# Kernel optimization log

Hardware: AMD Instinct MI355X
Metric: run time of the kernel (lower is better)

The kernel has to match this reference:

```python
import jax, jax.numpy as jnp
import numpy as np
from jax import lax

B, D, H, W, C = 2, 144, 64, 160, 32
P = 300000
EPS = 1e-4   # scn BatchNormLeakyReLU default eps
LEAK = 0.2


def setup_inputs() -> dict:
    key = jax.random.key(0)
    ks = jax.random.split(key, 10)
    features = jax.random.normal(ks[0], (P, C), jnp.float32)
    b = jax.random.randint(ks[1], (P, 1), 0, B)
    x = jax.random.randint(ks[2], (P, 1), 0, D)
    y = jax.random.randint(ks[3], (P, 1), 0, H)
    z = jax.random.randint(ks[4], (P, 1), 0, W)
    coords = jnp.concatenate([b, x, y, z], axis=1).astype(jnp.int32)

    def conv_w(k, cin, cout):
        return jax.random.normal(k, (2, 2, 2, cin, cout), jnp.float32) / np.float32(np.sqrt(8 * cin))

    return {
        "features": features, "coords": coords,
        "w1": conv_w(ks[5], C, 64),  "g1": jnp.ones((64,), jnp.float32),  "b1": jnp.zeros((64,), jnp.float32),
        "w2": conv_w(ks[6], 64, 96), "g2": jnp.ones((96,), jnp.float32),  "b2": jnp.zeros((96,), jnp.float32),
        "w3": conv_w(ks[7], 96, 128),"g3": jnp.ones((128,), jnp.float32), "b3": jnp.zeros((128,), jnp.float32),
        "w4": conv_w(ks[8], 128, 1),
    }


def _densify(features, coords):
    # scn.InputLayer mode=4: average features of duplicate coordinates.
    lin = ((coords[:, 0] * D + coords[:, 1]) * H + coords[:, 2]) * W + coords[:, 3]
    grid = jnp.zeros((B * D * H * W, C), features.dtype).at[lin].add(features)
    cnt = jnp.zeros((B * D * H * W,), features.dtype).at[lin].add(1.0)
    grid = grid / jnp.maximum(cnt, 1.0)[:, None]
    x = grid.reshape(B, D, H, W, C)
    mask = (cnt > 0).astype(features.dtype).reshape(B, D, H, W, 1)
    return x, mask


def _conv2s2(x, w):
    # scn.Convolution(dim=3, filter=2, stride=2, bias=False): inactive inputs are zero,
    # so dense VALID conv reproduces values at active output sites exactly.
    return lax.conv_general_dilated(x, w, (2, 2, 2), 'VALID',
                                    dimension_numbers=('NDHWC', 'DHWIO', 'NDHWC'))


def _downsample_mask(mask):
    # Output site is active iff any input in its 2x2x2 window is active.
    return lax.reduce_window(mask, 0.0, lax.max, (1, 2, 2, 2, 1), (1, 2, 2, 2, 1), 'VALID')


def _block(x, mask, w, gamma, beta):
    x = _conv2s2(x, w)
    mask = _downsample_mask(mask)
    n = jnp.maximum(jnp.sum(mask), 1.0)
    # x is exactly zero at inactive sites, so sums over all sites == sums over active sites.
    mean = jnp.sum(x, axis=(0, 1, 2, 3)) / n
    var = jnp.sum(x * x, axis=(0, 1, 2, 3)) / n - mean * mean
    y = (x - mean) * (gamma * lax.rsqrt(var + EPS)) + beta
    y = jnp.where(y > 0, y, LEAK * y) * mask   # LeakyReLU on active sites, zero elsewhere
    return y, mask


def reference(features, coords, w1, g1, b1, w2, g2, b2, w3, g3, b3, w4):
    x, mask = _densify(features, coords)
    x, mask = _block(x, mask, w1, g1, b1)
    x, mask = _block(x, mask, w2, g2, b2)
    x, mask = _block(x, mask, w3, g3, b3)
    x = _conv2s2(x, w4)                 # [B, 9, 4, 10, 1]
    mask = _downsample_mask(mask)
    return jax.nn.sigmoid(x) * mask     # sigmoid of features; inactive sites zeroed
```

## Files before the change

kernel.cpp:

```cpp
#include <hip/hip_runtime.h>
#include <math.h>

#define PNUM 300000
#define B_ 2
#define D0 144
#define H0 64
#define W0 160
#define NVOX (B_*D0*H0*W0)

#define D1 72
#define H1 32
#define W1 80
#define N1S (B_*D1*H1*W1)

#define D2 36
#define H2 16
#define W2 40
#define N2S (B_*D2*H2*W2)

#define D3 18
#define H3 8
#define W3 20
#define N3S (B_*D3*H3*W3)

#define D4 9
#define H4 4
#define W4 10
#define N4S (B_*D4*H4*W4)

#define EPS_ 1e-4f
#define LEAK_ 0.2f

typedef __attribute__((ext_vector_type(8))) short v8s;
typedef __attribute__((ext_vector_type(4))) float v4f;

typedef unsigned short ushort_t;
typedef unsigned int uint_t;
typedef unsigned long long ull_t;

__device__ __forceinline__ ushort_t f2b(float f) {
  union { float f; uint_t u; } x; x.f = f;
  uint_t r = x.u + 0x7FFFu + ((x.u >> 16) & 1u);
  return (ushort_t)(r >> 16);
}
__device__ __forceinline__ float b2f(ushort_t h) {
  union { uint_t u; float f; } x; x.u = ((uint_t)h) << 16; return x.f;
}
__device__ __forceinline__ uint_t bn2(uint_t w, float s0, float h0, float s1, float h1,
                                      float msk) {
  float v0 = b2f((ushort_t)(w & 0xffff));
  float v1 = b2f((ushort_t)(w >> 16));
  v0 = fmaf(v0, s0, h0); v1 = fmaf(v1, s1, h1);
  v0 = fmaxf(v0, LEAK_ * v0) * msk;
  v1 = fmaxf(v1, LEAK_ * v1) * msk;
  return (uint_t)f2b(v0) | ((uint_t)f2b(v1) << 16);
}

template <int DD, int HH, int WW>
__device__ __forceinline__ int okey(int p) {
  int b = p / (DD*HH*WW); int r = p - b*(DD*HH*WW);
  int x = r / (HH*WW); r -= x*(HH*WW);
  int y = r / WW; int z = r - y*WW;
  return (((((b*(DD/2) + (x >> 1))*(HH/2) + (y >> 1))*(WW/2)) + (z >> 1)) << 3)
         | ((x & 1) << 2) | ((y & 1) << 1) | (z & 1);
}

#define OFF_CNT     0
#define OFF_STATS   2949120
#define OFF_CURSOR  2965504
#define OFF_SORTED  5914624
#define OFF_AKLIST  6214624
#define OFF_WT1     6514624
#define OFF_WT2     6522816
#define OFF_WT3     6555584
#define OFF_AFEATB  6621120
#define OFF_X1B     11421120
#define OFF_X2B     23217600
#define OFF_X3B     26166720
#define OFF_M1      26535360
#define OFF_M2      26904000
#define OFF_M3      26950080

#define ST_S1P  0
#define ST_Q1P  2560
#define ST_S2P  5120
#define ST_Q2P  7424
#define ST_S3P  9728
#define ST_Q3P  12032
#define ST_N2P  14336
#define ST_N3P  14368
#define ST_GCUR 14400
#define ST_PK   14404

__device__ __forceinline__ int voxkey(int b, int x, int y, int z) {
  int p = ((b*D1 + (x >> 1))*H1 + (y >> 1))*W1 + (z >> 1);
  int oct = ((x & 1) << 2) | ((y & 1) << 1) | (z & 1);
  return p*8 + oct;
}

#define NB_COUNT 1172
#define NB_PREPW 832
#define NB_STZ   16
__global__ __launch_bounds__(256) void k_front(
    const int* __restrict__ coords, int* __restrict__ cnt,
    const float* __restrict__ w1, const float* __restrict__ w2,
    const float* __restrict__ w3,
    ushort_t* __restrict__ wt1, ushort_t* __restrict__ wt2,
    ushort_t* __restrict__ wt3, float* __restrict__ stz) {
  int bb = blockIdx.x, t = threadIdx.x;
  if (bb < NB_COUNT) {
    int i = bb * 256 + t;
    if (i < PNUM) {
      int4 c = *(const int4*)(coords + i*4);
      atomicAdd(&cnt[voxkey(c.x, c.y, c.z, c.w)], 1);
    }
  } else if (bb < NB_COUNT + NB_PREPW) {
    int idx = (bb - NB_COUNT) * 256 + t;
    if (idx < 16384) {
      int c = idx >> 11, r = idx & 2047;
      int co = r >> 5, kk = r & 31;
      wt1[idx] = f2b(w1[(c*32 + kk)*64 + co]);
    } else if (idx < 16384 + 65536) {
      int i = idx - 16384;
      int c = i >> 12, r = i & 4095;
      int co = r >> 5, kk = r & 31;
      int k = c*32 + kk;
      wt2[i] = (co < 96) ? f2b(w2[k*96 + co]) : 0;
    } else {
      int i = idx - 81920;
      int c = i >> 12, r = i & 4095;
      int co = r >> 5, kk = r & 31;
      int k = c*32 + kk;
      int ch = k >> 7, ci = k & 127;
      wt3[i] = (ci < 96) ? f2b(w3[(ch*96 + ci)*128 + co]) : 0;
    }
  } else {
    int off = ((bb - NB_COUNT - NB_PREPW) * 256 + t) * 4;
    *(float4*)(stz + off) = make_float4(0.f, 0.f, 0.f, 0.f);
  }
}

__global__ __launch_bounds__(1024) void k_alloc(const int* __restrict__ cnt,
                                                int* __restrict__ cursor,
                                                float* __restrict__ m1b,
                                                int* __restrict__ aklist,
                                                int* __restrict__ gcur,
                                                ull_t* __restrict__ pkctr) {
  __shared__ ull_t wsum[16];
  __shared__ int slotBase;
  __shared__ ull_t pkBase;
  int t = threadIdx.x;
  int idx0 = blockIdx.x * 16384 + t * 16;
  int c[16];
  int tsum = 0;
#pragma unroll
  for (int j = 0; j < 4; j++) {
    int4 cv = *(const int4*)(cnt + idx0 + j*4);
    c[j*4+0] = cv.x; c[j*4+1] = cv.y; c[j*4+2] = cv.z; c[j*4+3] = cv.w;
    tsum += cv.x + cv.y + cv.z + cv.w;
  }
  uint_t m0 = 0, m1m = 0;
#pragma unroll
  for (int j = 0; j < 8; j++) { if (c[j] > 0) m0 |= (1u << j); }
#pragma unroll
  for (int j = 0; j < 8; j++) { if (c[8+j] > 0) m1m |= (1u << j); }
  int ck = __popc(m0) + __popc(m1m);
  int pa = ((m0 != 0) ? 1 : 0) + ((m1m != 0) ? 1 : 0);
  ull_t sv = ((ull_t)(uint_t)tsum << 32) | (ull_t)(uint_t)((pa << 16) | ck);
  int lane = t & 63, wid = t >> 6;
  ull_t incl = sv;
#pragma unroll
  for (int o = 1; o < 64; o <<= 1) {
    ull_t v = __shfl_up(incl, o);
    if (lane >= o) incl += v;
  }
  if (lane == 63) wsum[wid] = incl;
  __syncthreads();
  if (t == 0) {
    ull_t tot = 0;
#pragma unroll
    for (int w = 0; w < 16; w++) { ull_t v = wsum[w]; wsum[w] = tot; tot += v; }
    slotBase = atomicAdd(gcur, (int)(tot >> 32));
    uint_t pk = (uint_t)(tot & 0xffffffffULL);
    pkBase = atomicAdd(pkctr, ((ull_t)(pk >> 16) << 32) | (ull_t)(pk & 0xffff));
  }
  __syncthreads();
  ull_t excl = wsum[wid] + incl - sv;
  int st = slotBase + (int)(excl >> 32);
  uint_t pkl = (uint_t)(excl & 0xffffffffULL);
  int koff = (int)(pkBase & 0xffffffffULL) + (int)(pkl & 0xffff);
#pragma unroll
  for (int j = 0; j < 4; j++) {
    int4 sv2;
    sv2.x = st; st += c[j*4+0];
    sv2.y = st; st += c[j*4+1];
    sv2.z = st; st += c[j*4+2];
    sv2.w = st; st += c[j*4+3];
    *(int4*)(cursor + idx0 + j*4) = sv2;
  }
  int p0 = idx0 >> 3;
  m1b[okey<D1,H1,W1>(p0)]     = (m0 != 0) ? 1.f : 0.f;
  m1b[okey<D1,H1,W1>(p0 + 1)] = (m1m != 0) ? 1.f : 0.f;
  uint_t m = m0;
  while (m) { int i = __ffs(m) - 1; m &= m - 1; aklist[koff++] = p0*8 + i; }
  m = m1m;
  while (m) { int i = __ffs(m) - 1; m &= m - 1; aklist[koff++] = (p0 + 1)*8 + i; }
}

__global__ __launch_bounds__(256) void k_scatter(const int* __restrict__ coords,
                                                 int* __restrict__ cursor,
                                                 int* __restrict__ sorted) {
  int i = blockIdx.x * 256 + threadIdx.x;
  if (i >= PNUM) return;
  int4 c = *(const int4*)(coords + i*4);
  int slot = atomicAdd(&cursor[voxkey(c.x, c.y, c.z, c.w)], 1);
  sorted[slot] = i;
}

__global__ __launch_bounds__(256) void k_avg(const float* __restrict__ feat,
                                             const int* __restrict__ sorted,
                                             const int* __restrict__ cnt,
                                             const int* __restrict__ cursor,
                                             const int* __restrict__ aklist,
                                             const int* __restrict__ nactk,
                                             ushort_t* __restrict__ afb) {
  int gid = blockIdx.x * 256 + threadIdx.x;
  int j = gid >> 3;
  if (j >= nactk[0]) return;
  int key = aklist[j];
  int c = cnt[key];
  int s0 = cursor[key] - c;
  int q = (gid & 7) * 4;
  float4 acc = {0.f, 0.f, 0.f, 0.f};
  for (int i = 0; i < c; i++) {
    float4 v = *(const float4*)(feat + (size_t)sorted[s0 + i] * 32 + q);
    acc.x += v.x; acc.y += v.y; acc.z += v.z; acc.w += v.w;
  }
  float inv = 1.f / (float)c;
  uint2 o;
  o.x = (uint_t)f2b(acc.x*inv) | ((uint_t)f2b(acc.y*inv) << 16);
  o.y = (uint_t)f2b(acc.z*inv) | ((uint_t)f2b(acc.w*inv) << 16);
  *(uint2*)(afb + (size_t)s0 * 32 + q) = o;
}

__global__ __launch_bounds__(256) void k_conv1m(
    const ushort_t* __restrict__ afb, const int* __restrict__ cnt,
    const int* __restrict__ cursor, const ushort_t* __restrict__ wtg,
    ushort_t* __restrict__ x1b, float* __restrict__ sp, float* __restrict__ qp) {
  __shared__ __align__(16) ushort_t wlds[16384];
  __shared__ int cst[128*9];
  __shared__ int okl[128];
  __shared__ float redS[4][64], redQ[4][64];
  int t = threadIdx.x;
#pragma unroll
  for (int i = 0; i < 8; i++)
    ((uint4*)wlds)[t + i*256] = ((const uint4*)wtg)[t + i*256];
  if (t < 128) {
    int p = blockIdx.x * 128 + t;
    okl[t] = okey<D1,H1,W1>(p);
    const int4* cp = (const int4*)(cnt + (size_t)p*8);
    const int4* up = (const int4*)(cursor + (size_t)p*8);
    int4 c0 = cp[0], c1 = cp[1], u0 = up[0], u1 = up[1];
    cst[t*9 + 0] = (c0.x > 0) ? (u0.x - c0.x) : -1;
    cst[t*9 + 1] = (c0.y > 0) ? (u0.y - c0.y) : -1;
    cst[t*9 + 2] = (c0.z > 0) ? (u0.z - c0.z) : -1;
    cst[t*9 + 3] = (c0.w > 0) ? (u0.w - c0.w) : -1;
    cst[t*9 + 4] = (c1.x > 0) ? (u1.x - c1.x) : -1;
    cst[t*9 + 5] = (c1.y > 0) ? (u1.y - c1.y) : -1;
    cst[t*9 + 6] = (c1.z > 0) ? (u1.z - c1.z) : -1;
    cst[t*9 + 7] = (c1.w > 0) ? (u1.w - c1.w) : -1;
  }
  __syncthreads();
  int lane = t & 63, wv = t >> 6;
  int l15 = lane & 15, q = lane >> 4;
  int SB = wv * 32;
  v8s a[8][2];
#pragma unroll
  for (int c = 0; c < 8; c++) {
#pragma unroll
    for (int mt = 0; mt < 2; mt++) {
      int site = SB + mt*16 + l15;
      int sp2 = cst[site*9 + c];
      v8s av = {0,0,0,0,0,0,0,0};
      if (sp2 >= 0) av = *(const v8s*)(afb + (size_t)sp2*32 + q*8);
      a[c][mt] = av;
    }
  }
  v4f acc[2][4];
#pragma unroll
  for (int i = 0; i < 2; i++)
#pragma unroll
    for (int j = 0; j < 4; j++) acc[i][j] = (v4f){0.f, 0.f, 0.f, 0.f};
#pragma unroll
  for (int c = 0; c < 8; c++) {
    v8s b[4];
#pragma unroll
    for (int nt = 0; nt < 4; nt++)
      b[nt] = *(const v8s*)&wlds[c*2048 + (nt*16 + l15)*32 + q*8];
#pragma unroll
    for (int mt = 0; mt < 2; mt++)
#pragma unroll
      for (int nt = 0; nt < 4; nt++)
        acc[mt][nt] = __builtin_amdgcn_mfma_f32_16x16x32_bf16(a[c][mt], b[nt], acc[mt][nt], 0, 0, 0);
  }
  float ss[4] = {0,0,0,0}, sq[4] = {0,0,0,0};
#pragma unroll
  for (int mt = 0; mt < 2; mt++) {
#pragma unroll
    for (int nt = 0; nt < 4; nt++) {
#pragma unroll
      for (int r = 0; r < 4; r++) {
        int sl = SB + mt*16 + q*4 + r;
        ushort_t h = f2b(acc[mt][nt][r]);
        float v = b2f(h);
        x1b[(size_t)okl[sl]*64 + nt*16 + l15] = h;
        ss[nt] += v; sq[nt] += v*v;
      }
    }
  }
#pragma unroll
  for (int nt = 0; nt < 4; nt++) {
    float v1 = ss[nt], v2 = sq[nt];
    v1 += __shfl_xor(v1, 16); v1 += __shfl_xor(v1, 32);
    v2 += __shfl_xor(v2, 16); v2 += __shfl_xor(v2, 32);
    if (lane < 16) { redS[wv][nt*16 + l15] = v1; redQ[wv][nt*16 + l15] = v2; }
  }
  __syncthreads();
  if (t < 64) {
    float s = redS[0][t] + redS[1][t] + redS[2][t] + redS[3][t];
    float qq = redQ[0][t] + redQ[1][t] + redQ[2][t] + redQ[3][t];
    int row = (blockIdx.x & 31) * 80;
    atomicAdd(&sp[row + t], s);
    atomicAdd(&qp[row + t], qq);
  }
}

template <int CSTRIDE, int CIN_REAL, bool NINT, int NROW, int INSTR,
          int DO, int HO, int WO>
__global__ __launch_bounds__(256) void k_convm(
    const ushort_t* __restrict__ xin, const float* __restrict__ mprev,
    const ushort_t* __restrict__ wtg,
    const float* __restrict__ gam, const float* __restrict__ bet,
    const float* __restrict__ spin, const float* __restrict__ qpin,
    const void* __restrict__ ncnt, const float* __restrict__ npin,
    ushort_t* __restrict__ xout, float* __restrict__ osum, float* __restrict__ osq,
    float* __restrict__ mout, float* __restrict__ npart) {
  const int NCHUNK = CSTRIDE / 4;
  __shared__ __align__(16) float sc[CSTRIDE], sh[CSTRIDE];
  __shared__ float cmask[64*9];
  __shared__ int okl[64];
  __shared__ float redS[4][64], redQ[4][64];
  int t = threadIdx.x;
  if (t < CSTRIDE) {
    float scv = 0.f, shv = 0.f;
    if (t < CIN_REAL) {
      float n;
      if (NINT) n = fmaxf((float)((const int*)ncnt)[0], 1.0f);
      else {
        float nn = 0.f;
        for (int r = 0; r < 32; r++) nn += npin[r];
        n = fmaxf(nn, 1.0f);
      }
      float s1 = 0.f, q1 = 0.f;
      for (int r = 0; r < NROW; r++) { s1 += spin[r*INSTR + t]; q1 += qpin[r*INSTR + t]; }
      float mean = s1 / n;
      float var = q1 / n - mean * mean;
      float s = gam[t] * rsqrtf(var + EPS_);
      scv = s; shv = bet[t] - mean * s;
    }
    sc[t] = scv; sh[t] = shv;
  }
#pragma unroll
  for (int ii = 0; ii < 2; ii++) {
    int idx = t + ii*256;
    cmask[(idx >> 3)*9 + (idx & 7)] = mprev[(size_t)blockIdx.x * 512 + idx];
  }
  if (t < 64) okl[t] = okey<DO,HO,WO>(blockIdx.x * 64 + t);
  __syncthreads();
  int lane = t & 63, wv = t >> 6;
  int l15 = lane & 15, q = lane >> 4;
  int SB = (wv & 1) * 32, NB = (wv >> 1) * 64;
  size_t gbase = (size_t)blockIdx.x * 512;
  v4f acc[2][4];
#pragma unroll
  for (int i = 0; i < 2; i++)
#pragma unroll
    for (int j = 0; j < 4; j++) acc[i][j] = (v4f){0.f, 0.f, 0.f, 0.f};
  uint4 rawN[2]; float mskN[2]; v8s bN[4];
#pragma unroll
  for (int mt = 0; mt < 2; mt++) {
    int site = SB + mt*16 + l15;
    rawN[mt] = *(const uint4*)(xin + (gbase + site*8) * CSTRIDE + q*8);
    mskN[mt] = cmask[site*9];
  }
#pragma unroll
  for (int nt = 0; nt < 4; nt++)
    bN[nt] = *(const v8s*)(wtg + (NB + nt*16 + l15)*32 + q*8);
#pragma unroll
  for (int c = 0; c < NCHUNK; c++) {
    uint4 raw[2] = {rawN[0], rawN[1]};
    float mskc[2] = {mskN[0], mskN[1]};
    v8s b[4] = {bN[0], bN[1], bN[2], bN[3]};
    if (c + 1 < NCHUNK) {
      int ch1 = ((c+1) * 32) / CSTRIDE;
      int cio1 = ((c+1) * 32) % CSTRIDE + q * 8;
#pragma unroll
      for (int mt = 0; mt < 2; mt++) {
        int site = SB + mt*16 + l15;
        rawN[mt] = *(const uint4*)(xin + (gbase + site*8 + ch1) * CSTRIDE + cio1);
        mskN[mt] = cmask[site*9 + ch1];
      }
#pragma unroll
      for (int nt = 0; nt < 4; nt++)
        bN[nt] = *(const v8s*)(wtg + (size_t)(c+1)*4096 + (NB + nt*16 + l15)*32 + q*8);
    }
    int cio = (c * 32) % CSTRIDE + q * 8;
    float4 sc0 = *(const float4*)&sc[cio];
    float4 sc1 = *(const float4*)&sc[cio + 4];
    float4 sh0 = *(const float4*)&sh[cio];
    float4 sh1 = *(const float4*)&sh[cio + 4];
    v8s a[2];
#pragma unroll
    for (int mt = 0; mt < 2; mt++) {
      int4 pk;
      pk.x = (int)bn2(raw[mt].x, sc0.x, sh0.x, sc0.y, sh0.y, mskc[mt]);
      pk.y = (int)bn2(raw[mt].y, sc0.z, sh0.z, sc0.w, sh0.w, mskc[mt]);
      pk.z = (int)bn2(raw[mt].z, sc1.x, sh1.x, sc1.y, sh1.y, mskc[mt]);
      pk.w = (int)bn2(raw[mt].w, sc1.z, sh1.z, sc1.w, sh1.w, mskc[mt]);
      a[mt] = *(v8s*)&pk;
    }
#pragma unroll
    for (int mt = 0; mt < 2; mt++)
#pragma unroll
      for (int nt = 0; nt < 4; nt++)
        acc[mt][nt] = __builtin_amdgcn_mfma_f32_16x16x32_bf16(a[mt], b[nt], acc[mt][nt], 0, 0, 0);
  }
  float ss[4] = {0,0,0,0}, sq[4] = {0,0,0,0};
#pragma unroll
  for (int mt = 0; mt < 2; mt++) {
#pragma unroll
    for (int nt = 0; nt < 4; nt++) {
#pragma unroll
      for (int r = 0; r < 4; r++) {
        int sl = SB + mt*16 + q*4 + r;
        ushort_t h = f2b(acc[mt][nt][r]);
        float v = b2f(h);
        xout[(size_t)okl[sl]*128 + NB + nt*16 + l15] = h;
        ss[nt] += v; sq[nt] += v*v;
      }
    }
  }
  if (t < 64) {
    bool act = false;
#pragma unroll
    for (int ch = 0; ch < 8; ch++) act |= (cmask[t*9 + ch] > 0.f);
    mout[okl[t]] = act ? 1.f : 0.f;
    unsigned long long bal = __ballot(act);
    if (t == 0) atomicAdd(&npart[blockIdx.x & 31], (float)__popcll(bal));
  }
#pragma unroll
  for (int nt = 0; nt < 4; nt++) {
    float v1 = ss[nt], v2 = sq[nt];
    v1 += __shfl_xor(v1, 16); v1 += __shfl_xor(v1, 32);
    v2 += __shfl_xor(v2, 16); v2 += __shfl_xor(v2, 32);
    if (lane < 16) { redS[wv][nt*16 + l15] = v1; redQ[wv][nt*16 + l15] = v2; }
  }
  __syncthreads();
  if (t < 128) {
    float s, qq;
    if (t < 64) { s = redS[0][t] + redS[1][t]; qq = redQ[0][t] + redQ[1][t]; }
    else        { s = redS[2][t-64] + redS[3][t-64]; qq = redQ[2][t-64] + redQ[3][t-64]; }
    int row = (blockIdx.x & 15) * 144;
    atomicAdd(&osum[row + t], s);
    atomicAdd(&osq[row + t], qq);
  }
}

__global__ __launch_bounds__(256) void k_final(
    const ushort_t* __restrict__ x3b, const float* __restrict__ m3b,
    const float* __restrict__ w4, const float* __restrict__ gam,
    const float* __restrict__ bet, const float* __restrict__ spin,
    const float* __restrict__ qpin, const float* __restrict__ npin,
    float* __restrict__ out) {
  __shared__ float sc[128], sh[128];
  __shared__ float msk[8];
  __shared__ float red[256];
  int t = threadIdx.x;
  if (t < 128) {
    float nn = 0.f;
    for (int r = 0; r < 32; r++) nn += npin[r];
    float n = fmaxf(nn, 1.0f);
    float s1 = 0.f, q1 = 0.f;
    for (int r = 0; r < 16; r++) { s1 += spin[r*144 + t]; q1 += qpin[r*144 + t]; }
    float mean = s1 / n;
    float var = q1 / n - mean * mean;
    float s = gam[t] * rsqrtf(var + EPS_);
    sc[t] = s; sh[t] = bet[t] - mean * s;
  }
  int g = blockIdx.x;
  if (t < 8) msk[t] = m3b[g*8 + t];
  __syncthreads();
  float acc = 0.f;
#pragma unroll
  for (int ii = 0; ii < 4; ii++) {
    int k = t + ii*256;
    int ch = k >> 7, ci = k & 127;
    float v = b2f(x3b[(size_t)(g*8 + ch)*128 + ci]);
    v = v * sc[ci] + sh[ci];
    v = (v > 0.f ? v : LEAK_ * v) * msk[ch];
    acc += v * w4[k];
  }
  red[t] = acc;
  __syncthreads();
  if (t < 128) red[t] += red[t + 128];
  __syncthreads();
  if (t < 64) {
    float v = red[t] + red[t + 64];
#pragma unroll
    for (int off = 32; off > 0; off >>= 1) v += __shfl_down(v, off);
    if (t == 0) {
      float any = (msk[0] + msk[1] + msk[2] + msk[3] + msk[4] + msk[5] + msk[6] + msk[7]) > 0.f ? 1.f : 0.f;
      out[g] = any / (1.0f + expf(-v));
    }
  }
}

extern "C" void kernel_launch(void* const* d_in, const int* in_sizes, int n_in,
                              void* d_out, int out_size, void* d_ws, size_t ws_size,
                              hipStream_t stream) {
  (void)in_sizes; (void)n_in; (void)out_size; (void)ws_size;
  const float* feat = (const float*)d_in[0];
  const int*   crd  = (const int*)d_in[1];
  const float* w1 = (const float*)d_in[2];
  const float* g1 = (const float*)d_in[3];
  const float* b1 = (const float*)d_in[4];
  const float* w2 = (const float*)d_in[5];
  const float* g2 = (const float*)d_in[6];
  const float* b2 = (const float*)d_in[7];
  const float* w3 = (const float*)d_in[8];
  const float* g3 = (const float*)d_in[9];
  const float* b3 = (const float*)d_in[10];
  const float* w4 = (const float*)d_in[11];
  float* out = (float*)d_out;
  float* ws  = (float*)d_ws;

  int*      cnt    = (int*)(ws + OFF_CNT);
  float*    st     = ws + OFF_STATS;
  int*      cursor = (int*)(ws + OFF_CURSOR);
  int*      sorted = (int*)(ws + OFF_SORTED);
  int*      aklist = (int*)(ws + OFF_AKLIST);
  ushort_t* wt1g   = (ushort_t*)(ws + OFF_WT1);
  ushort_t* wt2g   = (ushort_t*)(ws + OFF_WT2);
  ushort_t* wt3g   = (ushort_t*)(ws + OFF_WT3);
  ushort_t* afb    = (ushort_t*)(ws + OFF_AFEATB);
  ushort_t* x1b    = (ushort_t*)(ws + OFF_X1B);
  ushort_t* x2b    = (ushort_t*)(ws + OFF_X2B);
  ushort_t* x3b    = (ushort_t*)(ws + OFF_X3B);
  float*    m1b    = ws + OFF_M1;
  float*    m2b    = ws + OFF_M2;
  float*    m3b    = ws + OFF_M3;
  ull_t*    pkctr  = (ull_t*)(st + ST_PK);
  int*      nactk  = (int*)(st + ST_PK);
  int*      nactp  = (int*)(st + ST_PK + 1);

  hipMemsetAsync(cnt, 0, (size_t)NVOX * sizeof(int), stream);

  k_front<<<NB_COUNT + NB_PREPW + NB_STZ, 256, 0, stream>>>(
      crd, cnt, w1, w2, w3, wt1g, wt2g, wt3g, st);
  k_alloc<<<NVOX / 16384, 1024, 0, stream>>>(cnt, cursor, m1b, aklist,
                                             (int*)(st + ST_GCUR), pkctr);
  k_scatter<<<(PNUM + 255) / 256, 256, 0, stream>>>(crd, cursor, sorted);
  k_avg<<<(PNUM * 8) / 256 + 1, 256, 0, stream>>>(feat, sorted, cnt, cursor, aklist,
                                                  nactk, afb);
  k_conv1m<<<N1S / 128, 256, 0, stream>>>(afb, cnt, cursor, wt1g, x1b,
                                          st + ST_S1P, st + ST_Q1P);
  k_convm<64, 64, true, 32, 80, D2,H2,W2><<<N2S / 64, 256, 0, stream>>>(
      x1b, m1b, wt2g, g1, b1, st + ST_S1P, st + ST_Q1P, (const void*)nactp, nullptr,
      x2b, st + ST_S2P, st + ST_Q2P, m2b, st + ST_N2P);
  k_convm<128, 96, false, 16, 144, D3,H3,W3><<<N3S / 64, 256, 0, stream>>>(
      x2b, m2b, wt3g, g2, b2, st + ST_S2P, st + ST_Q2P, nullptr, st + ST_N2P,
      x3b, st + ST_S3P, st + ST_Q3P, m3b, st + ST_N3P);
  k_final<<<N4S, 256, 0, stream>>>(x3b, m3b, w4, g3, b3,
                                   st + ST_S3P, st + ST_Q3P, st + ST_N3P, out);
}
```

Before: 245.7 us.

## Fuse feature averaging into scatter and only reduce duplicate voxels

The scatter kernel now writes each point's feature, pre-scaled by 1/count and packed to bf16, straight into its sorted slot. This removes the separate sorted-index array and the gather pass over all active voxels. A small follow-up kernel sums only the voxels holding more than one point, using a duplicate list built in the alloc scan. Conv1 also skips stores for fully inactive sites, and the later convs skip loads for masked-out inputs. The trade-off is that duplicate sums are now accumulated from bf16 values, which changes rounding, and each scatter thread writes a full 64-byte row.

New measurement: 244.2 us. About the same (-0.6%).

```diff
diff --git a/kernel.cpp b/kernel.cpp
--- a/kernel.cpp
+++ b/kernel.cpp
@@ -68,8 +68,7 @@
 #define OFF_CNT     0
 #define OFF_STATS   2949120
 #define OFF_CURSOR  2965504
-#define OFF_SORTED  5914624
-#define OFF_AKLIST  6214624
+#define OFF_DKLIST  5914624
 #define OFF_WT1     6514624
 #define OFF_WT2     6522816
 #define OFF_WT3     6555584
@@ -143,7 +142,7 @@
 __global__ __launch_bounds__(1024) void k_alloc(const int* __restrict__ cnt,
                                                 int* __restrict__ cursor,
                                                 float* __restrict__ m1b,
-                                                int* __restrict__ aklist,
+                                                int* __restrict__ dklist,
                                                 int* __restrict__ gcur,
                                                 ull_t* __restrict__ pkctr) {
   __shared__ ull_t wsum[16];
@@ -152,21 +151,22 @@
   int t = threadIdx.x;
   int idx0 = blockIdx.x * 16384 + t * 16;
   int c[16];
-  int tsum = 0;
+  int tsum = 0, dup = 0;
 #pragma unroll
   for (int j = 0; j < 4; j++) {
     int4 cv = *(const int4*)(cnt + idx0 + j*4);
     c[j*4+0] = cv.x; c[j*4+1] = cv.y; c[j*4+2] = cv.z; c[j*4+3] = cv.w;
     tsum += cv.x + cv.y + cv.z + cv.w;
   }
+#pragma unroll
+  for (int j = 0; j < 16; j++) dup += (c[j] > 1) ? 1 : 0;
   uint_t m0 = 0, m1m = 0;
 #pragma unroll
   for (int j = 0; j < 8; j++) { if (c[j] > 0) m0 |= (1u << j); }
 #pragma unroll
   for (int j = 0; j < 8; j++) { if (c[8+j] > 0) m1m |= (1u << j); }
-  int ck = __popc(m0) + __popc(m1m);
   int pa = ((m0 != 0) ? 1 : 0) + ((m1m != 0) ? 1 : 0);
-  ull_t sv = ((ull_t)(uint_t)tsum << 32) | (ull_t)(uint_t)((pa << 16) | ck);
+  ull_t sv = ((ull_t)(uint_t)tsum << 32) | (ull_t)(uint_t)((pa << 16) | dup);
   int lane = t & 63, wid = t >> 6;
   ull_t incl = sv;
 #pragma unroll
@@ -201,45 +201,58 @@
   int p0 = idx0 >> 3;
   m1b[okey<D1,H1,W1>(p0)]     = (m0 != 0) ? 1.f : 0.f;
   m1b[okey<D1,H1,W1>(p0 + 1)] = (m1m != 0) ? 1.f : 0.f;
-  uint_t m = m0;
-  while (m) { int i = __ffs(m) - 1; m &= m - 1; aklist[koff++] = p0*8 + i; }
-  m = m1m;
-  while (m) { int i = __ffs(m) - 1; m &= m - 1; aklist[koff++] = (p0 + 1)*8 + i; }
+#pragma unroll
+  for (int j = 0; j < 16; j++)
+    if (c[j] > 1) dklist[koff++] = idx0 + j;
 }
 
 __global__ __launch_bounds__(256) void k_scatter(const int* __restrict__ coords,
+                                                 const float* __restrict__ feat,
+                                                 const int* __restrict__ cnt,
                                                  int* __restrict__ cursor,
-                                                 int* __restrict__ sorted) {
+                                                 ushort_t* __restrict__ afb) {
   int i = blockIdx.x * 256 + threadIdx.x;
   if (i >= PNUM) return;
   int4 c = *(const int4*)(coords + i*4);
-  int slot = atomicAdd(&cursor[voxkey(c.x, c.y, c.z, c.w)], 1);
-  sorted[slot] = i;
-}
-
-__global__ __launch_bounds__(256) void k_avg(const float* __restrict__ feat,
-                                             const int* __restrict__ sorted,
-                                             const int* __restrict__ cnt,
-                                             const int* __restrict__ cursor,
-                                             const int* __restrict__ aklist,
-                                             const int* __restrict__ nactk,
-                                             ushort_t* __restrict__ afb) {
+  int key = voxkey(c.x, c.y, c.z, c.w);
+  int slot = atomicAdd(&cursor[key], 1);
+  float inv = 1.f / (float)cnt[key];
+  const float4* fp = (const float4*)(feat + (size_t)i * 32);
+  uint_t o[16];
+#pragma unroll
+  for (int q = 0; q < 8; q++) {
+    float4 v = fp[q];
+    o[q*2]   = (uint_t)f2b(v.x*inv) | ((uint_t)f2b(v.y*inv) << 16);
+    o[q*2+1] = (uint_t)f2b(v.z*inv) | ((uint_t)f2b(v.w*inv) << 16);
+  }
+  uint4* dst = (uint4*)(afb + (size_t)slot * 32);
+  dst[0] = make_uint4(o[0], o[1], o[2], o[3]);
+  dst[1] = make_uint4(o[4], o[5], o[6], o[7]);
+  dst[2] = make_uint4(o[8], o[9], o[10], o[11]);
+  dst[3] = make_uint4(o[12], o[13], o[14], o[15]);
+}
+
+__global__ __launch_bounds__(256) void k_davg(const int* __restrict__ cnt,
+                                              const int* __restrict__ cursor,
+                                              const int* __restrict__ dklist,
+                                              const int* __restrict__ ndup,
+                                              ushort_t* __restrict__ afb) {
   int gid = blockIdx.x * 256 + threadIdx.x;
   int j = gid >> 3;
-  if (j >= nactk[0]) return;
-  int key = aklist[j];
+  if (j >= ndup[0]) return;
+  int key = dklist[j];
   int c = cnt[key];
   int s0 = cursor[key] - c;
   int q = (gid & 7) * 4;
-  float4 acc = {0.f, 0.f, 0.f, 0.f};
+  float a0 = 0.f, a1 = 0.f, a2 = 0.f, a3 = 0.f;
   for (int i = 0; i < c; i++) {
-    float4 v = *(const float4*)(feat + (size_t)sorted[s0 + i] * 32 + q);
-    acc.x += v.x; acc.y += v.y; acc.z += v.z; acc.w += v.w;
-  }
-  float inv = 1.f / (float)c;
+    uint2 u = *(const uint2*)(afb + (size_t)(s0 + i) * 32 + q);
+    a0 += b2f((ushort_t)(u.x & 0xffff)); a1 += b2f((ushort_t)(u.x >> 16));
+    a2 += b2f((ushort_t)(u.y & 0xffff)); a3 += b2f((ushort_t)(u.y >> 16));
+  }
   uint2 o;
-  o.x = (uint_t)f2b(acc.x*inv) | ((uint_t)f2b(acc.y*inv) << 16);
-  o.y = (uint_t)f2b(acc.z*inv) | ((uint_t)f2b(acc.w*inv) << 16);
+  o.x = (uint_t)f2b(a0) | ((uint_t)f2b(a1) << 16);
+  o.y = (uint_t)f2b(a2) | ((uint_t)f2b(a3) << 16);
   *(uint2*)(afb + (size_t)s0 * 32 + q) = o;
 }
 
@@ -250,6 +263,7 @@
   __shared__ __align__(16) ushort_t wlds[16384];
   __shared__ int cst[128*9];
   __shared__ int okl[128];
+  __shared__ int pact[128];
   __shared__ float redS[4][64], redQ[4][64];
   int t = threadIdx.x;
 #pragma unroll
@@ -269,6 +283,7 @@
     cst[t*9 + 5] = (c1.y > 0) ? (u1.y - c1.y) : -1;
     cst[t*9 + 6] = (c1.z > 0) ? (u1.z - c1.z) : -1;
     cst[t*9 + 7] = (c1.w > 0) ? (u1.w - c1.w) : -1;
+    pact[t] = (c0.x + c0.y + c0.z + c0.w + c1.x + c1.y + c1.z + c1.w) > 0 ? 1 : 0;
   }
   __syncthreads();
   int lane = t & 63, wv = t >> 6;
@@ -313,7 +328,7 @@
         int sl = SB + mt*16 + q*4 + r;
         ushort_t h = f2b(acc[mt][nt][r]);
         float v = b2f(h);
-        x1b[(size_t)okl[sl]*64 + nt*16 + l15] = h;
+        if (pact[sl]) x1b[(size_t)okl[sl]*64 + nt*16 + l15] = h;
         ss[nt] += v; sq[nt] += v*v;
       }
     }
@@ -390,8 +405,10 @@
 #pragma unroll
   for (int mt = 0; mt < 2; mt++) {
     int site = SB + mt*16 + l15;
-    rawN[mt] = *(const uint4*)(xin + (gbase + site*8) * CSTRIDE + q*8);
-    mskN[mt] = cmask[site*9];
+    float m = cmask[site*9];
+    uint4 rv = make_uint4(0, 0, 0, 0);
+    if (m > 0.f) rv = *(const uint4*)(xin + (gbase + site*8) * CSTRIDE + q*8);
+    rawN[mt] = rv; mskN[mt] = m;
   }
 #pragma unroll
   for (int nt = 0; nt < 4; nt++)
@@ -407,8 +424,10 @@
 #pragma unroll
       for (int mt = 0; mt < 2; mt++) {
         int site = SB + mt*16 + l15;
-        rawN[mt] = *(const uint4*)(xin + (gbase + site*8 + ch1) * CSTRIDE + cio1);
-        mskN[mt] = cmask[site*9 + ch1];
+        float m = cmask[site*9 + ch1];
+        uint4 rv = make_uint4(0, 0, 0, 0);
+        if (m > 0.f) rv = *(const uint4*)(xin + (gbase + site*8 + ch1) * CSTRIDE + cio1);
+        rawN[mt] = rv; mskN[mt] = m;
       }
 #pragma unroll
       for (int nt = 0; nt < 4; nt++)
@@ -547,8 +566,7 @@
   int*      cnt    = (int*)(ws + OFF_CNT);
   float*    st     = ws + OFF_STATS;
   int*      cursor = (int*)(ws + OFF_CURSOR);
-  int*      sorted = (int*)(ws + OFF_SORTED);
-  int*      aklist = (int*)(ws + OFF_AKLIST);
+  int*      dklist = (int*)(ws + OFF_DKLIST);
   ushort_t* wt1g   = (ushort_t*)(ws + OFF_WT1);
   ushort_t* wt2g   = (ushort_t*)(ws + OFF_WT2);
   ushort_t* wt3g   = (ushort_t*)(ws + OFF_WT3);
@@ -560,18 +578,17 @@
   float*    m2b    = ws + OFF_M2;
   float*    m3b    = ws + OFF_M3;
   ull_t*    pkctr  = (ull_t*)(st + ST_PK);
-  int*      nactk  = (int*)(st + ST_PK);
+  int*      ndup   = (int*)(st + ST_PK);
   int*      nactp  = (int*)(st + ST_PK + 1);
 
   hipMemsetAsync(cnt, 0, (size_t)NVOX * sizeof(int), stream);
 
   k_front<<<NB_COUNT + NB_PREPW + NB_STZ, 256, 0, stream>>>(
       crd, cnt, w1, w2, w3, wt1g, wt2g, wt3g, st);
-  k_alloc<<<NVOX / 16384, 1024, 0, stream>>>(cnt, cursor, m1b, aklist,
+  k_alloc<<<NVOX / 16384, 1024, 0, stream>>>(cnt, cursor, m1b, dklist,
                                              (int*)(st + ST_GCUR), pkctr);
-  k_scatter<<<(PNUM + 255) / 256, 256, 0, stream>>>(crd, cursor, sorted);
-  k_avg<<<(PNUM * 8) / 256 + 1, 256, 0, stream>>>(feat, sorted, cnt, cursor, aklist,
-                                                  nactk, afb);
+  k_scatter<<<(PNUM + 255) / 256, 256, 0, stream>>>(crd, feat, cnt, cursor, afb);
+  k_davg<<<4688, 256, 0, stream>>>(cnt, cursor, dklist, ndup, afb);
   k_conv1m<<<N1S / 128, 256, 0, stream>>>(afb, cnt, cursor, wt1g, x1b,
                                           st + ST_S1P, st + ST_Q1P);
   k_convm<64, 64, true, 32, 80, D2,H2,W2><<<N2S / 64, 256, 0, stream>>>(
```
